# Optimization experiments

Hardware: AMD Instinct MI355X
Metric: run time of the kernel (lower is better)

## Reference

```python
import jax, jax.numpy as jnp
import numpy as np

B, S, D = 8, 2048, 256
C, H = 32, 4
HD = D // H  # head_dim = 64


def setup_inputs() -> dict:
    key = jax.random.key(0)
    ks = jax.random.split(key, 12)
    scale = 0.02
    x = jax.random.normal(ks[0], (B, S, D), dtype=jnp.float32)
    conditioning = jax.random.uniform(ks[1], (B, S, C), dtype=jnp.float32)
    Wq_w = jax.random.normal(ks[2], (D, D), dtype=jnp.float32) * scale
    Wq_b = jax.random.normal(ks[3], (D,), dtype=jnp.float32) * scale
    Wv_w = jax.random.normal(ks[4], (D, D), dtype=jnp.float32) * scale
    Wv_b = jax.random.normal(ks[5], (D,), dtype=jnp.float32) * scale
    Wk_w = jax.random.normal(ks[6], (C, D, D), dtype=jnp.float32) * scale  # stacked per-class torch Linear weights [out,in]
    Wk_b = jax.random.normal(ks[7], (C, D), dtype=jnp.float32) * scale
    Wo_w = jax.random.normal(ks[8], (D, D), dtype=jnp.float32) * scale
    Wo_b = jax.random.normal(ks[9], (D,), dtype=jnp.float32) * scale
    return {"x": x, "conditioning": conditioning,
            "Wq_w": Wq_w, "Wq_b": Wq_b, "Wv_w": Wv_w, "Wv_b": Wv_b,
            "Wk_w": Wk_w, "Wk_b": Wk_b, "Wo_w": Wo_w, "Wo_b": Wo_b}


def reference(x, conditioning, Wq_w, Wq_b, Wv_w, Wv_b, Wk_w, Wk_b, Wo_w, Wo_b):
    # torch Linear: y = x @ W.T + b, with W of shape [out, in]
    q = (x @ Wq_w.T + Wq_b).reshape(B, S, H, HD).transpose(0, 2, 1, 3)  # (B,H,S,HD)
    v = (x @ Wv_w.T + Wv_b).reshape(B, S, H, HD).transpose(0, 2, 1, 3)
    # per-class keys: (B,C,S,D)
    class_keys = jnp.einsum('bsd,cfd->bcsf', x, Wk_w) + Wk_b[None, :, None, :]
    # data-dependent weighted sum over classes -> effective key (B,S,D)
    k = jnp.einsum('bsc,bcsf->bsf', conditioning, class_keys)
    k = k.reshape(B, S, H, HD).transpose(0, 2, 1, 3)  # (B,H,S,HD)
    # scaled dot-product attention (dropout_p = 0)
    scale = 1.0 / jnp.sqrt(jnp.float32(HD))
    scores = jnp.einsum('bhqd,bhkd->bhqk', q, k) * scale
    attn = jax.nn.softmax(scores, axis=-1)
    out = jnp.einsum('bhqk,bhkd->bhqd', attn, v)
    out = out.transpose(0, 2, 1, 3).reshape(B, S, D)
    return out @ Wo_w.T + Wo_b
```

## Files before the change

kernel.cpp:

```cpp
#include <hip/hip_runtime.h>
#include <hip/hip_bf16.h>

#define BB 8
#define SS 2048
#define DD 256
#define CC 32
#define HH 4
#define HD 64
#define MTOT (BB*SS)

using bf16    = __hip_bfloat16;
using short8  = __attribute__((ext_vector_type(8))) short;
using short4v = __attribute__((ext_vector_type(4))) short;
using floatx4 = __attribute__((ext_vector_type(4))) float;

#if __has_builtin(__builtin_amdgcn_mfma_f32_16x16x16_bf16)
  #define MFMA_PV16(a,b,c) __builtin_amdgcn_mfma_f32_16x16x16_bf16(a,b,c,0,0,0)
  #define HAVE_PV16 1
#elif __has_builtin(__builtin_amdgcn_mfma_f32_16x16x16bf16_1k)
  #define MFMA_PV16(a,b,c) __builtin_amdgcn_mfma_f32_16x16x16bf16_1k(a,b,c,0,0,0)
  #define HAVE_PV16 1
#else
  #define HAVE_PV16 0
#endif

#if __has_builtin(__builtin_amdgcn_global_load_lds)
  #define HAVE_GLL 1
#else
  #define HAVE_GLL 0
#endif

__device__ inline float bf2f(unsigned short u) {
    union { unsigned int i; float f; } v; v.i = ((unsigned int)u) << 16; return v.f;
}
__device__ inline unsigned short f2bfbits(float f) {
    bf16 h = __float2bfloat16(f);
    return __builtin_bit_cast(unsigned short, h);
}

#define N_X    (MTOT*DD)
#define N_COND (MTOT*CC)
#define N_WQW  (DD*DD)
#define N_WQB  (DD)
#define N_WVW  (DD*DD)
#define N_WVB  (DD)
#define N_WKW  (CC*DD*DD)
#define N_WKB  (CC*DD)
#define N_WOW  (DD*DD)
#define N_WOB  (DD)
#define P0 0
#define P1 (P0+N_X)
#define P2 (P1+N_COND)
#define P3 (P2+N_WQW)
#define P4 (P3+N_WQB)
#define P5 (P4+N_WVW)
#define P6 (P5+N_WVB)
#define P7 (P6+N_WKW)
#define P8 (P7+N_WKB)
#define P9 (P8+N_WOW)
#define PTOT (P9+N_WOB)

__global__ void convert_all(const void* s0, const void* s1, const void* s2,
                            const void* s3, const void* s4, const void* s5,
                            const void* s6, const void* s7, const void* s8,
                            const void* s9, bf16* dst, int* flagw)
{
    __shared__ int cnts[4];
    {
        const float* xf = (const float*)s0;
        float v = fabsf(xf[threadIdx.x]);
        bool ok = (v == v) && v > 1e-4f && v < 1e4f;
        unsigned long long m = __ballot(ok);
        if ((threadIdx.x & 63) == 0) cnts[threadIdx.x >> 6] = __popcll(m);
    }
    __syncthreads();
    const bool f32 = (cnts[0] + cnts[1] + cnts[2] + cnts[3]) > 128;
    if (blockIdx.x == 0 && threadIdx.x == 0) *flagw = f32 ? 1 : 0;

    size_t i = ((size_t)blockIdx.x * 256 + threadIdx.x) * 8;
    const size_t stride = (size_t)gridDim.x * 256 * 8;
    for (; i < (size_t)PTOT; i += stride) {
        const void* src; size_t off;
        if      (i < P1) { src = s0; off = i - P0; }
        else if (i < P2) { src = s1; off = i - P1; }
        else if (i < P3) { src = s2; off = i - P2; }
        else if (i < P4) { src = s3; off = i - P3; }
        else if (i < P5) { src = s4; off = i - P4; }
        else if (i < P6) { src = s5; off = i - P5; }
        else if (i < P7) { src = s6; off = i - P6; }
        else if (i < P8) { src = s7; off = i - P7; }
        else if (i < P9) { src = s8; off = i - P8; }
        else             { src = s9; off = i - P9; }
        if (f32) {
            const float* s = (const float*)src + off;
            float4 a = *(const float4*)(s);
            float4 b = *(const float4*)(s + 4);
            __align__(16) unsigned short t[8];
            t[0] = f2bfbits(a.x); t[1] = f2bfbits(a.y);
            t[2] = f2bfbits(a.z); t[3] = f2bfbits(a.w);
            t[4] = f2bfbits(b.x); t[5] = f2bfbits(b.y);
            t[6] = f2bfbits(b.z); t[7] = f2bfbits(b.w);
            *(uint4*)(dst + i) = *(const uint4*)t;
        } else {
            *(uint4*)(dst + i) = *(const uint4*)((const unsigned short*)src + off);
        }
    }
}

__device__ __forceinline__ void gemm_body(const bf16* __restrict__ X, const bf16* __restrict__ W,
                                          const bf16* __restrict__ bias, void* __restrict__ Yv,
                                          const int* __restrict__ flagp, int flex_out, int vt_out,
                                          unsigned short* smem, int m0, int n0)
{
    const int LDT = 264;
    unsigned short* xs = smem;
    unsigned short* ws = smem + 64 * 264;
    const int t = threadIdx.x;

    for (int i = 0; i < 8; ++i) {
        int c = t + i * 256;
        int row = c >> 5, col = (c & 31) * 8;
        *(uint4*)&xs[row * LDT + col] = *(const uint4*)(X + (size_t)(m0 + row) * DD + col);
        *(uint4*)&ws[row * LDT + col] = *(const uint4*)(W + (size_t)(n0 + row) * DD + col);
    }
    __syncthreads();

    const int w = t >> 6, lane = t & 63;
    const int lrow = lane & 15, lk = (lane >> 4) * 8, rgrp = (lane >> 4) * 4;
    floatx4 acc[4] = {};
    const unsigned short* ax = &xs[(w * 16 + lrow) * LDT + lk];
    for (int kt = 0; kt < 8; ++kt) {
        short8 a = *(const short8*)(ax + kt * 32);
        #pragma unroll
        for (int j = 0; j < 4; ++j) {
            short8 b = *(const short8*)&ws[(j * 16 + lrow) * LDT + kt * 32 + lk];
            acc[j] = __builtin_amdgcn_mfma_f32_16x16x32_bf16(a, b, acc[j], 0, 0, 0);
        }
    }

    if (vt_out) {
        __syncthreads();
        unsigned short* ts = xs;
        #pragma unroll
        for (int j = 0; j < 4; ++j) {
            float bv = __bfloat162float(bias[n0 + j * 16 + lrow]);
            #pragma unroll
            for (int r = 0; r < 4; ++r)
                ts[(j * 16 + lrow) * 72 + w * 16 + rgrp + r] = f2bfbits(acc[j][r] + bv);
        }
        __syncthreads();
        const int bq = m0 >> 11, s0v = m0 & 2047, h = n0 >> 6;
        bf16* dstb = (bf16*)Yv + ((size_t)(bq * HH + h) * HD) * SS + s0v;
        for (int i = 0; i < 2; ++i) {
            int idx = t + i * 256, row = idx >> 3, ch = (idx & 7) * 8;
            *(uint4*)(dstb + (size_t)row * SS + ch) = *(const uint4*)&ts[row * 72 + ch];
        }
        return;
    }

    const bool f32o = flex_out && (*flagp != 0);
    #pragma unroll
    for (int j = 0; j < 4; ++j) {
        int col = n0 + j * 16 + lrow;
        float bv = __bfloat162float(bias[col]);
        #pragma unroll
        for (int r = 0; r < 4; ++r) {
            int row = m0 + w * 16 + rgrp + r;
            float val = acc[j][r] + bv;
            if (f32o) ((float*)Yv)[(size_t)row * DD + col] = val;
            else      ((bf16*)Yv)[(size_t)row * DD + col] = __float2bfloat16(val);
        }
    }
}

__launch_bounds__(256, 2)
__global__ void gemm_qv(const bf16* __restrict__ X,
                        const bf16* __restrict__ Wqw, const bf16* __restrict__ Wqb, bf16* __restrict__ Qout,
                        const bf16* __restrict__ Wvw, const bf16* __restrict__ Wvb, bf16* __restrict__ Vout,
                        const int* __restrict__ flagp)
{
    __shared__ __align__(16) unsigned short smem[2 * 64 * 264];
    int gi = blockIdx.x;
    if (gi < 1024) {
        int n0 = (gi & 3) * 64, m0 = (gi >> 2) * 64;
        gemm_body(X, Wqw, Wqb, (void*)Qout, flagp, 0, 0, smem, m0, n0);
    } else {
        gi -= 1024;
        int n0 = (gi & 3) * 64, m0 = (gi >> 2) * 64;
        gemm_body(X, Wvw, Wvb, (void*)Vout, flagp, 0, 1, smem, m0, n0);
    }
}

__launch_bounds__(256, 2)
__global__ void gemm_bias(const bf16* __restrict__ X, const bf16* __restrict__ W,
                          const bf16* __restrict__ bias, void* __restrict__ Yv,
                          const int* __restrict__ flagp, int flex_out, int vt_out)
{
    __shared__ __align__(16) unsigned short smem[2 * 64 * 264];
    gemm_body(X, W, bias, Yv, flagp, flex_out, vt_out, smem, blockIdx.y * 64, blockIdx.x * 64);
}

__device__ __forceinline__ void stage_ws4(const bf16* __restrict__ Wc,
                                          unsigned short* wsbuf, int w, int lane)
{
    #pragma unroll
    for (int i = 0; i < 8; ++i) {
        int rr = w * 16 + i * 2 + (lane >> 5);
        int cs = (lane & 31) ^ (rr & 7);
        const bf16* src = Wc + (size_t)rr * DD + cs * 8;
        unsigned short* dst = wsbuf + (size_t)(w * 16 + i * 2) * DD;
#if HAVE_GLL
        __builtin_amdgcn_global_load_lds(
            (const __attribute__((address_space(1))) void*)src,
            (__attribute__((address_space(3))) void*)dst, 16, 0, 0);
#else
        uint4 v = *(const uint4*)src;
        *(uint4*)(dst + (size_t)lane * 8) = v;
#endif
    }
}

__launch_bounds__(256, 2)
__global__ void classkey(const bf16* __restrict__ X, const bf16* __restrict__ Cond,
                         const bf16* __restrict__ Wk, const bf16* __restrict__ Wkb,
                         bf16* __restrict__ Kout)
{
    __shared__ __align__(16) unsigned short ws[2][64 * 256];
    __shared__ __align__(16) unsigned short conds[128 * 32];
    __shared__ __align__(16) unsigned short kbs[32 * 64];
    const int t    = threadIdx.x;
    const int w    = t >> 6;
    const int lane = t & 63;
    const int r16  = lane & 15;
    const int quad = lane >> 4;
    const int m0   = blockIdx.y * 128;
    const int n0   = blockIdx.x * 64;

    #pragma unroll
    for (int i = 0; i < 2; ++i) {
        int chunk = t + i * 256;
        int row = chunk >> 2, c8 = (chunk & 3) * 8;
        *(uint4*)&conds[row * 32 + c8] = *(const uint4*)(Cond + (size_t)(m0 + row) * CC + c8);
    }
    {
        int row = t >> 3, c8 = (t & 7) * 8;
        *(uint4*)&kbs[row * 64 + c8] = *(const uint4*)(Wkb + (size_t)row * DD + n0 + c8);
    }

    short8 xa[2][8];
    #pragma unroll
    for (int mt = 0; mt < 2; ++mt) {
        const bf16* xrow = X + (size_t)(m0 + w * 32 + mt * 16 + r16) * DD + quad * 8;
        #pragma unroll
        for (int kt = 0; kt < 8; ++kt)
            xa[mt][kt] = *(const short8*)(xrow + kt * 32);
    }

    stage_ws4(Wk + (size_t)n0 * DD, &ws[0][0], w, lane);

    floatx4 acck[2][4] = {};
    for (int c = 0; c < CC; ++c) {
        __syncthreads();
        if (c + 1 < CC)
            stage_ws4(Wk + (size_t)(c + 1) * DD * DD + (size_t)n0 * DD,
                      &ws[(c + 1) & 1][0], w, lane);

        const unsigned short* wb = &ws[c & 1][0];
        floatx4 p[2][4] = {};
        #pragma unroll
        for (int kt = 0; kt < 8; ++kt) {
            short8 bj[4];
            #pragma unroll
            for (int j = 0; j < 4; ++j)
                bj[j] = *(const short8*)&wb[(j * 16 + r16) * DD +
                                            (((kt * 4 + quad) ^ (r16 & 7)) << 3)];
            #pragma unroll
            for (int mt = 0; mt < 2; ++mt)
                #pragma unroll
                for (int j = 0; j < 4; ++j)
                    p[mt][j] = __builtin_amdgcn_mfma_f32_16x16x32_bf16(xa[mt][kt], bj[j], p[mt][j], 0, 0, 0);
        }
        #pragma unroll
        for (int mt = 0; mt < 2; ++mt)
            #pragma unroll
            for (int r = 0; r < 4; ++r) {
                float cv = bf2f(conds[(w * 32 + mt * 16 + quad * 4 + r) * 32 + c]);
                #pragma unroll
                for (int j = 0; j < 4; ++j) acck[mt][j][r] += cv * p[mt][j][r];
            }
    }

    float kbv[2][4][4] = {};
    for (int c = 0; c < CC; ++c) {
        #pragma unroll
        for (int mt = 0; mt < 2; ++mt)
            #pragma unroll
            for (int r = 0; r < 4; ++r) {
                float cf = bf2f(conds[(w * 32 + mt * 16 + quad * 4 + r) * 32 + c]);
                #pragma unroll
                for (int j = 0; j < 4; ++j)
                    kbv[mt][j][r] += cf * bf2f(kbs[c * 64 + j * 16 + r16]);
            }
    }
    #pragma unroll
    for (int mt = 0; mt < 2; ++mt)
        #pragma unroll
        for (int j = 0; j < 4; ++j) {
            int col = n0 + j * 16 + r16;
            #pragma unroll
            for (int r = 0; r < 4; ++r) {
                int row = m0 + w * 32 + mt * 16 + quad * 4 + r;
                Kout[(size_t)row * DD + col] = __float2bfloat16(acck[mt][j][r] + kbv[mt][j][r]);
            }
        }
}

__device__ inline void stage_kv(const bf16* __restrict__ kRow,
                                const bf16* __restrict__ vRow,
                                unsigned short* kbuf, unsigned short* vbuf,
                                int w, int lane)
{
    int r  = w * 8 + (lane >> 3);
    int cs = (lane & 7) ^ (r & 7);
#if HAVE_GLL
    __builtin_amdgcn_global_load_lds(
        (const __attribute__((address_space(1))) void*)(kRow + (size_t)r * DD + cs * 8),
        (__attribute__((address_space(3))) void*)(kbuf + w * 512), 16, 0, 0);
    __builtin_amdgcn_global_load_lds(
        (const __attribute__((address_space(1))) void*)(vRow + (size_t)r * SS + cs * 8),
        (__attribute__((address_space(3))) void*)(vbuf + w * 512), 16, 0, 0);
#else
    *(uint4*)(kbuf + w * 512 + (size_t)lane * 8) = *(const uint4*)(kRow + (size_t)r * DD + cs * 8);
    *(uint4*)(vbuf + w * 512 + (size_t)lane * 8) = *(const uint4*)(vRow + (size_t)r * SS + cs * 8);
#endif
}

__launch_bounds__(512, 4)
__global__ void attn(const bf16* __restrict__ Q, const bf16* __restrict__ Kb,
                     const bf16* __restrict__ VT, bf16* __restrict__ O)
{
    __shared__ __align__(16) unsigned short ks[2][64 * 64];
    __shared__ __align__(16) unsigned short vt[2][64 * 64];
#if !HAVE_PV16
    __shared__ __align__(16) unsigned short ps[128 * 72];
#endif
    const int t    = threadIdx.x;
    const int w    = t >> 6;
    const int lane = t & 63;
    const int r16  = lane & 15;
    const int quad = lane >> 4;
    const int bh   = blockIdx.y;
    const int b    = bh >> 2, h = bh & 3;
    const int q0   = blockIdx.x * 128;
    const size_t base  = ((size_t)b * SS) * DD + h * HD;
    const size_t vbase = (size_t)bh * HD * SS;

    short8 qa[2];
    {
        const bf16* qrow = Q + base + (size_t)(q0 + w * 16 + r16) * DD + quad * 8;
        #pragma unroll
        for (int k2 = 0; k2 < 2; ++k2) {
            short8 raw = *(const short8*)(qrow + k2 * 32);
            short8 sc;
            #pragma unroll
            for (int e = 0; e < 8; ++e)
                sc[e] = (short)f2bfbits(bf2f((unsigned short)raw[e]) * 0.125f);
            qa[k2] = sc;
        }
    }

    stage_kv(Kb + base, VT + vbase, &ks[0][0], &vt[0][0], w, lane);

    floatx4 acco[4] = {};
    float mrun = -1e30f, lrun = 0.f;

    for (int kt = 0; kt < SS / 64; ++kt) {
        __syncthreads();
        if (kt + 1 < SS / 64)
            stage_kv(Kb + base + (size_t)(kt + 1) * 64 * DD,
                     VT + vbase + (size_t)(kt + 1) * 64,
                     &ks[(kt + 1) & 1][0], &vt[(kt + 1) & 1][0], w, lane);

        const unsigned short* kbuf = &ks[kt & 1][0];
        const unsigned short* vbuf = &vt[kt & 1][0];

        floatx4 s[4] = {};
        #pragma unroll
        for (int k2 = 0; k2 < 2; ++k2) {
            short8 bq = qa[k2];
            #pragma unroll
            for (int j = 0; j < 4; ++j) {
                short8 ak = *(const short8*)&kbuf[(j * 16 + r16) * 64 +
                                                  (((k2 * 4 + quad) ^ (r16 & 7)) << 3)];
                s[j] = __builtin_amdgcn_mfma_f32_16x16x32_bf16(ak, bq, s[j], 0, 0, 0);
            }
        }

        float mx = -1e30f;
        #pragma unroll
        for (int j = 0; j < 4; ++j)
            #pragma unroll
            for (int r = 0; r < 4; ++r) mx = fmaxf(mx, s[j][r]);
        mx = fmaxf(mx, __shfl_xor(mx, 16, 64));
        mx = fmaxf(mx, __shfl_xor(mx, 32, 64));
        float mnew  = fmaxf(mrun, mx);
        float alpha = __expf(mrun - mnew);
        float sum = 0.f;
        #pragma unroll
        for (int j = 0; j < 4; ++j)
            #pragma unroll
            for (int r = 0; r < 4; ++r) {
                float e = __expf(s[j][r] - mnew);
                s[j][r] = e; sum += e;
            }
        sum += __shfl_xor(sum, 16, 64);
        sum += __shfl_xor(sum, 32, 64);
        lrun = lrun * alpha + sum;
        mrun = mnew;

        #pragma unroll
        for (int r = 0; r < 4; ++r) {
            float ar = __shfl(alpha, (quad << 4) + quad * 4 + r, 64);
            #pragma unroll
            for (int jn = 0; jn < 4; ++jn) acco[jn][r] *= ar;
        }

#if HAVE_PV16
        #pragma unroll
        for (int j = 0; j < 4; ++j) {
            short4v p;
            p[0] = (short)f2bfbits(s[j][0]); p[1] = (short)f2bfbits(s[j][1]);
            p[2] = (short)f2bfbits(s[j][2]); p[3] = (short)f2bfbits(s[j][3]);
            #pragma unroll
            for (int jn = 0; jn < 4; ++jn) {
                short4v vv = *(const short4v*)&vbuf[(jn * 16 + r16) * 64 +
                                                    ((((j * 2) + (quad >> 1)) ^ (r16 & 7)) << 3) +
                                                    (quad & 1) * 4];
                acco[jn] = MFMA_PV16(p, vv, acco[jn]);
            }
        }
#else
        #pragma unroll
        for (int j = 0; j < 4; ++j)
            #pragma unroll
            for (int r = 0; r < 4; ++r)
                ps[(w * 16 + r16) * 72 + j * 16 + quad * 4 + r] = f2bfbits(s[j][r]);
        #pragma unroll
        for (int k2 = 0; k2 < 2; ++k2) {
            short8 a = *(const short8*)&ps[(w * 16 + r16) * 72 + k2 * 32 + quad * 8];
            #pragma unroll
            for (int jn = 0; jn < 4; ++jn) {
                short8 bb = *(const short8*)&vbuf[(jn * 16 + r16) * 64 +
                                                  (((k2 * 4 + quad) ^ (r16 & 7)) << 3)];
                acco[jn] = __builtin_amdgcn_mfma_f32_16x16x32_bf16(a, bb, acco[jn], 0, 0, 0);
            }
        }
#endif
    }

    #pragma unroll
    for (int r = 0; r < 4; ++r) {
        float lr = __shfl(lrun, (quad << 4) + quad * 4 + r, 64);
        float inv = 1.0f / lr;
        int row = q0 + w * 16 + quad * 4 + r;
        #pragma unroll
        for (int jn = 0; jn < 4; ++jn)
            O[base + (size_t)row * DD + jn * 16 + r16] = __float2bfloat16(acco[jn][r] * inv);
    }
}

extern "C" void kernel_launch(void* const* d_in, const int* in_sizes, int n_in,
                              void* d_out, int out_size, void* d_ws, size_t ws_size,
                              hipStream_t stream)
{
    int*  flag = (int*)d_ws;
    bf16* conv = (bf16*)((char*)d_ws + 256);

    const bf16* xb    = conv + P0;
    const bf16* condb = conv + P1;
    const bf16* wqw   = conv + P2;
    const bf16* wqb   = conv + P3;
    const bf16* wvw   = conv + P4;
    const bf16* wvb   = conv + P5;
    const bf16* wkw   = conv + P6;
    const bf16* wkb   = conv + P7;
    const bf16* wow   = conv + P8;
    const bf16* wob   = conv + P9;

    bf16* qb = conv + PTOT;
    bf16* kb = qb + (size_t)MTOT * DD;
    bf16* vb = kb + (size_t)MTOT * DD;
    bf16* ob = vb + (size_t)MTOT * DD;

    dim3 blk(256);
    hipLaunchKernelGGL(convert_all, dim3((PTOT / 8 + 255) / 256), blk, 0, stream,
                       d_in[0], d_in[1], d_in[2], d_in[3], d_in[4],
                       d_in[5], d_in[6], d_in[7], d_in[8], d_in[9],
                       conv, flag);

    dim3 gck(DD / 64, MTOT / 128);
    hipLaunchKernelGGL(classkey, gck, blk, 0, stream, xb, condb, wkw, wkb, kb);

    hipLaunchKernelGGL(gemm_qv, dim3(2048), blk, 0, stream,
                       xb, wqw, wqb, qb, wvw, wvb, vb, flag);

    dim3 ga(SS / 128, BB * HH);
    hipLaunchKernelGGL(attn, ga, dim3(512), 0, stream, qb, kb, vb, ob);

    dim3 gg(DD / 64, MTOT / 64);
    hipLaunchKernelGGL(gemm_bias, gg, blk, 0, stream, ob, wow, wob, d_out, flag, 1, 0);
}
```

Before: 250.7 us.

## Split classkey K-dimension across warps, fold bias via MFMA, coalesce output stores

```diff
diff --git a/kernel.cpp b/kernel.cpp
--- a/kernel.cpp
+++ b/kernel.cpp
@@ -220,99 +220,132 @@
     }
 }
 
+#define WS_HALF (64 * 256)
+#define CONDS_OFF 65536
+#define KBST_OFF  75776
+#define SMEM_BYTES 80896
+
 __launch_bounds__(256, 2)
 __global__ void classkey(const bf16* __restrict__ X, const bf16* __restrict__ Cond,
                          const bf16* __restrict__ Wk, const bf16* __restrict__ Wkb,
                          bf16* __restrict__ Kout)
 {
-    __shared__ __align__(16) unsigned short ws[2][64 * 256];
-    __shared__ __align__(16) unsigned short conds[128 * 32];
-    __shared__ __align__(16) unsigned short kbs[32 * 64];
+    __shared__ __align__(16) unsigned char smem[SMEM_BYTES];
+    unsigned short* wsbase = (unsigned short*)smem;
+    unsigned short* conds  = (unsigned short*)(smem + CONDS_OFF);
+    unsigned short* kbsT   = (unsigned short*)(smem + KBST_OFF);
+
     const int t    = threadIdx.x;
     const int w    = t >> 6;
     const int lane = t & 63;
     const int r16  = lane & 15;
     const int quad = lane >> 4;
+    const int mw   = w & 1;
+    const int kw   = w >> 1;
     const int m0   = blockIdx.y * 128;
     const int n0   = blockIdx.x * 64;
 
+    {
+        int row = t >> 1, c16 = (t & 1) * 16;
+        *(uint4*)&conds[row * 40 + c16]     = *(const uint4*)(Cond + (size_t)(m0 + row) * CC + c16);
+        *(uint4*)&conds[row * 40 + c16 + 8] = *(const uint4*)(Cond + (size_t)(m0 + row) * CC + c16 + 8);
+    }
+    {
+        int f = t >> 2, cbase = (t & 3) * 8;
+        #pragma unroll
+        for (int e = 0; e < 8; ++e)
+            kbsT[f * 40 + cbase + e] =
+                __builtin_bit_cast(unsigned short, Wkb[(size_t)(cbase + e) * DD + n0 + f]);
+    }
+
+    short8 xa[4][4];
     #pragma unroll
-    for (int i = 0; i < 2; ++i) {
-        int chunk = t + i * 256;
-        int row = chunk >> 2, c8 = (chunk & 3) * 8;
-        *(uint4*)&conds[row * 32 + c8] = *(const uint4*)(Cond + (size_t)(m0 + row) * CC + c8);
-    }
-    {
-        int row = t >> 3, c8 = (t & 7) * 8;
-        *(uint4*)&kbs[row * 64 + c8] = *(const uint4*)(Wkb + (size_t)row * DD + n0 + c8);
-    }
-
-    short8 xa[2][8];
-    #pragma unroll
-    for (int mt = 0; mt < 2; ++mt) {
-        const bf16* xrow = X + (size_t)(m0 + w * 32 + mt * 16 + r16) * DD + quad * 8;
-        #pragma unroll
-        for (int kt = 0; kt < 8; ++kt)
+    for (int mt = 0; mt < 4; ++mt) {
+        const bf16* xrow = X + (size_t)(m0 + mw * 64 + mt * 16 + r16) * DD + kw * 128 + quad * 8;
+        #pragma unroll
+        for (int kt = 0; kt < 4; ++kt)
             xa[mt][kt] = *(const short8*)(xrow + kt * 32);
     }
 
-    stage_ws4(Wk + (size_t)n0 * DD, &ws[0][0], w, lane);
-
-    floatx4 acck[2][4] = {};
+    stage_ws4(Wk + (size_t)n0 * DD, wsbase, w, lane);
+
+    floatx4 acck[4][4] = {};
     for (int c = 0; c < CC; ++c) {
         __syncthreads();
         if (c + 1 < CC)
             stage_ws4(Wk + (size_t)(c + 1) * DD * DD + (size_t)n0 * DD,
-                      &ws[(c + 1) & 1][0], w, lane);
-
-        const unsigned short* wb = &ws[c & 1][0];
-        floatx4 p[2][4] = {};
-        #pragma unroll
-        for (int kt = 0; kt < 8; ++kt) {
+                      wsbase + ((c + 1) & 1) * WS_HALF, w, lane);
+
+        const unsigned short* wb = wsbase + (c & 1) * WS_HALF;
+        floatx4 p[4][4];
+        #pragma unroll
+        for (int kt = 0; kt < 4; ++kt) {
             short8 bj[4];
             #pragma unroll
             for (int j = 0; j < 4; ++j)
                 bj[j] = *(const short8*)&wb[(j * 16 + r16) * DD +
-                                            (((kt * 4 + quad) ^ (r16 & 7)) << 3)];
-            #pragma unroll
-            for (int mt = 0; mt < 2; ++mt)
+                          (((kw * 16 + kt * 4 + quad) ^ (r16 & 7)) << 3)];
+            if (kt == 0) {
+                floatx4 z = {};
                 #pragma unroll
-                for (int j = 0; j < 4; ++j)
-                    p[mt][j] = __builtin_amdgcn_mfma_f32_16x16x32_bf16(xa[mt][kt], bj[j], p[mt][j], 0, 0, 0);
-        }
-        #pragma unroll
-        for (int mt = 0; mt < 2; ++mt)
+                for (int mt = 0; mt < 4; ++mt)
+                    #pragma unroll
+                    for (int j = 0; j < 4; ++j)
+                        p[mt][j] = __builtin_amdgcn_mfma_f32_16x16x32_bf16(xa[mt][0], bj[j], z, 0, 0, 0);
+            } else {
+                #pragma unroll
+                for (int mt = 0; mt < 4; ++mt)
+                    #pragma unroll
+                    for (int j = 0; j < 4; ++j)
+                        p[mt][j] = __builtin_amdgcn_mfma_f32_16x16x32_bf16(xa[mt][kt], bj[j], p[mt][j], 0, 0, 0);
+            }
+        }
+        #pragma unroll
+        for (int mt = 0; mt < 4; ++mt)
             #pragma unroll
             for (int r = 0; r < 4; ++r) {
-                float cv = bf2f(conds[(w * 32 + mt * 16 + quad * 4 + r) * 32 + c]);
+                float cv = bf2f(conds[(mw * 64 + mt * 16 + quad * 4 + r) * 40 + c]);
                 #pragma unroll
                 for (int j = 0; j < 4; ++j) acck[mt][j][r] += cv * p[mt][j][r];
             }
     }
 
-    float kbv[2][4][4] = {};
-    for (int c = 0; c < CC; ++c) {
-        #pragma unroll
-        for (int mt = 0; mt < 2; ++mt)
-            #pragma unroll
-            for (int r = 0; r < 4; ++r) {
-                float cf = bf2f(conds[(w * 32 + mt * 16 + quad * 4 + r) * 32 + c]);
-                #pragma unroll
-                for (int j = 0; j < 4; ++j)
-                    kbv[mt][j][r] += cf * bf2f(kbs[c * 64 + j * 16 + r16]);
-            }
-    }
+    if (kw == 0) {
+        #pragma unroll
+        for (int mt = 0; mt < 4; ++mt) {
+            short8 ac = *(const short8*)&conds[(mw * 64 + mt * 16 + r16) * 40 + quad * 8];
+            #pragma unroll
+            for (int j = 0; j < 4; ++j) {
+                short8 bc = *(const short8*)&kbsT[(j * 16 + r16) * 40 + quad * 8];
+                acck[mt][j] = __builtin_amdgcn_mfma_f32_16x16x32_bf16(ac, bc, acck[mt][j], 0, 0, 0);
+            }
+        }
+    }
+
+    float* red = (float*)smem;
+    __syncthreads();
     #pragma unroll
-    for (int mt = 0; mt < 2; ++mt)
-        #pragma unroll
-        for (int j = 0; j < 4; ++j) {
-            int col = n0 + j * 16 + r16;
-            #pragma unroll
-            for (int r = 0; r < 4; ++r) {
-                int row = m0 + w * 32 + mt * 16 + quad * 4 + r;
-                Kout[(size_t)row * DD + col] = __float2bfloat16(acck[mt][j][r] + kbv[mt][j][r]);
-            }
-        }
+    for (int mt = 0; mt < 4; ++mt)
+        #pragma unroll
+        for (int j = 0; j < 4; ++j)
+            #pragma unroll
+            for (int r = 0; r < 4; ++r)
+                red[(kw * 128 + mw * 64 + mt * 16 + quad * 4 + r) * 65 + j * 16 + r16] =
+                    acck[mt][j][r];
+    __syncthreads();
+    {
+        int row = t >> 1, cg = (t & 1) * 32;
+        __align__(16) unsigned short outv[32];
+        #pragma unroll
+        for (int cc = 0; cc < 32; ++cc) {
+            float s = red[(size_t)row * 65 + cg + cc] + red[(size_t)(128 + row) * 65 + cg + cc];
+            outv[cc] = f2bfbits(s);
+        }
+        bf16* dst = Kout + (size_t)(m0 + row) * DD + n0 + cg;
+        #pragma unroll
+        for (int u = 0; u < 4; ++u)
+            *(uint4*)(dst + u * 8) = *(const uint4*)&outv[u * 8];
+    }
 }
 
 __device__ inline void stage_kv(const bf16* __restrict__ kRow,
```

Result: faster. 244.2 us (-2.6%).
